# Kernel tuning notes

Measured on AMD Instinct MI355X. Metric: run time of the kernel, lower is better.

The kernel has to match this reference:

```python
import jax, jax.numpy as jnp
import numpy as np

B, S, D_MODEL, H = 2, 2048, 2048, 16
HEAD_DIM = D_MODEL // H  # 128


def setup_inputs() -> dict:
    key = jax.random.key(0)
    k1, k2, k3 = jax.random.split(key, 3)
    x = jax.random.normal(k1, (B, S, D_MODEL), dtype=jnp.float32)
    Wqkv = jax.random.normal(k2, (D_MODEL, 3 * D_MODEL), dtype=jnp.float32) * (D_MODEL ** -0.5)
    Wout = jax.random.normal(k3, (D_MODEL, D_MODEL), dtype=jnp.float32) * (D_MODEL ** -0.5)
    return {"x": x, "Wqkv": Wqkv, "Wout": Wout}


def reference(x, Wqkv, Wout):
    b, s, _ = x.shape
    # QKV projection: (B, S, 3*H*D) -> (B, S, 3, H, D)
    qkv = (x @ Wqkv).reshape(b, s, 3, H, HEAD_DIM)
    q, k, v = qkv[:, :, 0], qkv[:, :, 1], qkv[:, :, 2]
    scale = HEAD_DIM ** -0.5
    # scores: (B, H, Sq, Sk)
    scores = jnp.einsum("bqhd,bkhd->bhqk", q, k) * scale
    causal = jnp.arange(s)[:, None] >= jnp.arange(s)[None, :]
    scores = jnp.where(causal[None, None, :, :], scores, -1e9)
    attn = jax.nn.softmax(scores, axis=-1)
    out = jnp.einsum("bhqk,bkhd->bqhd", attn, v)  # (B, S, H, D)
    out = out.reshape(b, s, D_MODEL)
    return out @ Wout
```

## Files before the change

### kernel.cpp

```cpp
#include <hip/hip_runtime.h>
#include <hip/hip_bf16.h>


#define SEQ 2048
#define DM 2048
#define NQKV 6144
#define DH 128

typedef __attribute__((ext_vector_type(8))) short bf16x8;
typedef __attribute__((ext_vector_type(4))) float f32x4;

__device__ __forceinline__ f32x4 mfma16(bf16x8 a, bf16x8 b, f32x4 c) {
  return __builtin_amdgcn_mfma_f32_16x16x32_bf16(a, b, c, 0, 0, 0);
}

__device__ __forceinline__ void gload_lds16(const void* g, void* l) {
  __builtin_amdgcn_global_load_lds(
      (const __attribute__((address_space(1))) unsigned int*)g,
      (__attribute__((address_space(3))) unsigned int*)l, 16, 0, 0);
}

__global__ __launch_bounds__(256) void cast_f32_bf16(
    const float* __restrict__ in, __hip_bfloat16* __restrict__ out, int n4) {
  int i = blockIdx.x * 256 + threadIdx.x;
  if (i >= n4) return;
  float4 f = reinterpret_cast<const float4*>(in)[i];
  union { __hip_bfloat16 h[4]; unsigned long long u; } o;
  o.h[0] = __float2bfloat16(f.x); o.h[1] = __float2bfloat16(f.y);
  o.h[2] = __float2bfloat16(f.z); o.h[3] = __float2bfloat16(f.w);
  reinterpret_cast<unsigned long long*>(out)[i] = o.u;
}

__global__ __launch_bounds__(256) void transpose_cast(
    const float* __restrict__ in, __hip_bfloat16* __restrict__ out, int R, int C) {
  __shared__ float t[32][33];
  int c0 = blockIdx.x * 32, r0 = blockIdx.y * 32;
  int tx = threadIdx.x, ty = threadIdx.y;
#pragma unroll
  for (int i = 0; i < 4; ++i)
    t[ty + i * 8][tx] = in[(size_t)(r0 + ty + i * 8) * C + c0 + tx];
  __syncthreads();
#pragma unroll
  for (int i = 0; i < 4; ++i)
    out[(size_t)(c0 + ty + i * 8) * R + r0 + tx] = __float2bfloat16(t[tx][ty + i * 8]);
}

__global__ __launch_bounds__(256) void transpose_v(
    const __hip_bfloat16* __restrict__ qkv, __hip_bfloat16* __restrict__ vT) {
  __shared__ __hip_bfloat16 t[32][33];
  int bh = blockIdx.z;
  int b = bh >> 4, h = bh & 15;
  int s0 = blockIdx.x * 32, d0 = blockIdx.y * 32;
  int tx = threadIdx.x, ty = threadIdx.y;
#pragma unroll
  for (int i = 0; i < 4; ++i)
    t[ty + i * 8][tx] =
        qkv[(size_t)(b * SEQ + s0 + ty + i * 8) * NQKV + 2 * DM + h * DH + d0 + tx];
  __syncthreads();
#pragma unroll
  for (int i = 0; i < 4; ++i)
    vT[(size_t)(bh * DH + d0 + ty + i * 8) * SEQ + s0 + tx] = t[tx][ty + i * 8];
}

template <int EPI>
__global__ __launch_bounds__(256) void gemm_bt(
    const __hip_bfloat16* __restrict__ A, const __hip_bfloat16* __restrict__ Bt,
    void* __restrict__ Cout, int M, int N, int K) {
  __shared__ alignas(16) __hip_bfloat16 As[128 * 64];
  __shared__ alignas(16) __hip_bfloat16 Bs[128 * 64];
  const int tid = threadIdx.x;
  const int lane = tid & 63;
  const int w = tid >> 6, wr = w >> 1, wc = w & 1;
  const int lr = lane & 15, lg = lane >> 4;
  const int m0 = blockIdx.y * 128, n0 = blockIdx.x * 128;
  f32x4 acc[4][4] = {};
  for (int k0 = 0; k0 < K; k0 += 64) {
#pragma unroll
    for (int it = 0; it < 4; ++it) {
      int e = (it * 256 + tid) * 8;
      int row = e >> 6, col = e & 63;
      gload_lds16(A + (size_t)(m0 + row) * K + k0 + col, (char*)As + (size_t)e * 2);
      gload_lds16(Bt + (size_t)(n0 + row) * K + k0 + col, (char*)Bs + (size_t)e * 2);
    }
    __syncthreads();
#pragma unroll
    for (int ks = 0; ks < 2; ++ks) {
      bf16x8 af[4], bfr[4];
#pragma unroll
      for (int m = 0; m < 4; ++m)
        af[m] = *(const bf16x8*)((const char*)As +
                                 (wr * 64 + m * 16 + lr) * 128 + ks * 64 + lg * 16);
#pragma unroll
      for (int n = 0; n < 4; ++n)
        bfr[n] = *(const bf16x8*)((const char*)Bs +
                                  (wc * 64 + n * 16 + lr) * 128 + ks * 64 + lg * 16);
#pragma unroll
      for (int m = 0; m < 4; ++m)
#pragma unroll
        for (int n = 0; n < 4; ++n)
          acc[m][n] = mfma16(af[m], bfr[n], acc[m][n]);
    }
    __syncthreads();
  }
  const int crow = m0 + wr * 64, ccol = n0 + wc * 64;
#pragma unroll
  for (int m = 0; m < 4; ++m)
#pragma unroll
    for (int n = 0; n < 4; ++n)
#pragma unroll
      for (int j = 0; j < 4; ++j) {
        int r = crow + m * 16 + lg * 4 + j;
        int c = ccol + n * 16 + lr;
        if (EPI == 0)
          ((__hip_bfloat16*)Cout)[(size_t)r * N + c] = __float2bfloat16(acc[m][n][j]);
        else
          ((float*)Cout)[(size_t)r * N + c] = acc[m][n][j];
      }
}

__global__ __launch_bounds__(256) void attn_causal(
    const __hip_bfloat16* __restrict__ qkv, const __hip_bfloat16* __restrict__ vT,
    __hip_bfloat16* __restrict__ O) {
  __shared__ alignas(16) __hip_bfloat16 Ks[64 * 128];
  __shared__ alignas(16) __hip_bfloat16 Vs[128 * 64];
  __shared__ alignas(16) __hip_bfloat16 Ps[4][16 * 64];
  const int tid = threadIdx.x, lane = tid & 63, w = tid >> 6;
  const int lr = lane & 15, lg = lane >> 4;
  const int qt = blockIdx.x, bh = blockIdx.y;
  const int b = bh >> 4, h = bh & 15;
  const int q0 = qt * 64;
  const int qrow = q0 + w * 16 + lr;
  const __hip_bfloat16* qp = qkv + (size_t)(b * SEQ + qrow) * NQKV + h * DH;
  bf16x8 qf[4];
#pragma unroll
  for (int ks = 0; ks < 4; ++ks) qf[ks] = *(const bf16x8*)(qp + ks * 32 + lg * 8);
  f32x4 of[8] = {};
  float mrun[4], lrun[4];
#pragma unroll
  for (int j = 0; j < 4; ++j) { mrun[j] = -1e30f; lrun[j] = 0.f; }
  const float scale = 0.08838834764831845f;
  const int myq = q0 + w * 16 + lg * 4;

  for (int t = 0; t <= qt; ++t) {
    const int kv0 = t * 64;
#pragma unroll
    for (int it = 0; it < 4; ++it) {
      int g = it * 256 + tid;
      int r = g >> 4, sl = g & 15;
      int ssl = sl ^ (r & 7);
      gload_lds16(qkv + (size_t)(b * SEQ + kv0 + r) * NQKV + DM + h * DH + ssl * 8,
                  (char*)Ks + (size_t)g * 16);
    }
#pragma unroll
    for (int it = 0; it < 4; ++it) {
      int g = it * 256 + tid;
      int r = g >> 3, sl = g & 7;
      int ssl = sl ^ (r & 7);
      gload_lds16(vT + (size_t)(bh * DH + r) * SEQ + kv0 + ssl * 8,
                  (char*)Vs + (size_t)g * 16);
    }
    __syncthreads();

    f32x4 sacc[4] = {};
#pragma unroll
    for (int n = 0; n < 4; ++n) {
      const int krow = n * 16 + lr;
      const char* kbase = (const char*)Ks + krow * 256;
#pragma unroll
      for (int ks = 0; ks < 4; ++ks) {
        int c = ks * 64 + lg * 16;
        bf16x8 kb = *(const bf16x8*)(kbase + (c ^ ((krow & 7) << 4)));
        sacc[n] = mfma16(qf[ks], kb, sacc[n]);
      }
    }
    const bool dg = (t == qt);
#pragma unroll
    for (int n = 0; n < 4; ++n)
#pragma unroll
      for (int j = 0; j < 4; ++j) {
        float v = sacc[n][j] * scale;
        if (dg && (kv0 + n * 16 + lr > myq + j)) v = -1e30f;
        sacc[n][j] = v;
      }
    float pm[4];
#pragma unroll
    for (int j = 0; j < 4; ++j)
      pm[j] = fmaxf(fmaxf(sacc[0][j], sacc[1][j]), fmaxf(sacc[2][j], sacc[3][j]));
#pragma unroll
    for (int d = 1; d < 16; d <<= 1)
#pragma unroll
      for (int j = 0; j < 4; ++j) pm[j] = fmaxf(pm[j], __shfl_xor(pm[j], d));
    float corr[4], rs[4];
#pragma unroll
    for (int j = 0; j < 4; ++j) {
      float mn = fmaxf(mrun[j], pm[j]);
      corr[j] = __expf(mrun[j] - mn);
      mrun[j] = mn;
      rs[j] = 0.f;
    }
#pragma unroll
    for (int n = 0; n < 4; ++n)
#pragma unroll
      for (int j = 0; j < 4; ++j) {
        float p = __expf(sacc[n][j] - mrun[j]);
        sacc[n][j] = p;
        rs[j] += p;
      }
#pragma unroll
    for (int d = 1; d < 16; d <<= 1)
#pragma unroll
      for (int j = 0; j < 4; ++j) rs[j] += __shfl_xor(rs[j], d);
#pragma unroll
    for (int j = 0; j < 4; ++j) lrun[j] = lrun[j] * corr[j] + rs[j];
#pragma unroll
    for (int nn = 0; nn < 8; ++nn)
#pragma unroll
      for (int j = 0; j < 4; ++j) of[nn][j] *= corr[j];

    __hip_bfloat16* pw = &Ps[w][0];
#pragma unroll
    for (int j = 0; j < 4; ++j) {
      int prow = lg * 4 + j;
      char* pb = (char*)pw + prow * 128;
#pragma unroll
      for (int n = 0; n < 4; ++n) {
        int c = (n * 16 + lr) * 2;
        *(__hip_bfloat16*)(pb + (c ^ ((prow & 7) << 4))) = __float2bfloat16(sacc[n][j]);
      }
    }
#pragma unroll
    for (int kvs = 0; kvs < 2; ++kvs) {
      int c = kvs * 64 + lg * 16;
      bf16x8 pa = *(const bf16x8*)((const char*)pw + lr * 128 + (c ^ ((lr & 7) << 4)));
#pragma unroll
      for (int nn = 0; nn < 8; ++nn) {
        int vrow = nn * 16 + lr;
        bf16x8 vb =
            *(const bf16x8*)((const char*)Vs + vrow * 128 + (c ^ ((vrow & 7) << 4)));
        of[nn] = mfma16(pa, vb, of[nn]);
      }
    }
    __syncthreads();
  }
#pragma unroll
  for (int j = 0; j < 4; ++j) {
    float inv = 1.0f / lrun[j];
    size_t orow = (size_t)(b * SEQ + q0 + w * 16 + lg * 4 + j);
    __hip_bfloat16* op = O + orow * DM + h * DH;
#pragma unroll
    for (int nn = 0; nn < 8; ++nn)
      op[nn * 16 + lr] = __float2bfloat16(of[nn][j] * inv);
  }
}

extern "C" void kernel_launch(void* const* d_in, const int* in_sizes, int n_in,
                              void* d_out, int out_size, void* d_ws, size_t ws_size,
                              hipStream_t stream) {
  const float* x = (const float*)d_in[0];
  const float* Wqkv = (const float*)d_in[1];
  const float* Wout = (const float*)d_in[2];
  float* out = (float*)d_out;
  char* ws = (char*)d_ws;
  __hip_bfloat16* xb    = (__hip_bfloat16*)(ws + 0);
  __hip_bfloat16* wqkvT = (__hip_bfloat16*)(ws + (size_t)16777216);
  __hip_bfloat16* woutT = (__hip_bfloat16*)(ws + (size_t)41943040);
  __hip_bfloat16* qkvb  = (__hip_bfloat16*)(ws + (size_t)50331648);
  __hip_bfloat16* vT    = (__hip_bfloat16*)(ws + (size_t)100663296);
  __hip_bfloat16* ob    = (__hip_bfloat16*)(ws + (size_t)117440512);

  cast_f32_bf16<<<dim3(8192), dim3(256), 0, stream>>>(x, xb, 8388608 / 4);
  transpose_cast<<<dim3(192, 64), dim3(32, 8), 0, stream>>>(Wqkv, wqkvT, 2048, 6144);
  transpose_cast<<<dim3(64, 64), dim3(32, 8), 0, stream>>>(Wout, woutT, 2048, 2048);
  gemm_bt<0><<<dim3(48, 32), dim3(256), 0, stream>>>(xb, wqkvT, qkvb, 4096, 6144, 2048);
  transpose_v<<<dim3(64, 4, 32), dim3(32, 8), 0, stream>>>(qkvb, vT);
  attn_causal<<<dim3(32, 32), dim3(256), 0, stream>>>(qkvb, vT, ob);
  gemm_bt<1><<<dim3(16, 32), dim3(256), 0, stream>>>(ob, woutT, out, 4096, 2048, 2048);
}
```

Baseline: 507.3 us.

## Pair causal query tiles per block, widen KV tiles, add lazy rescale

Each attention block now handles two query tiles (p and 31-p), so the causal work is balanced across blocks and each K/V tile loaded into LDS is shared by both query tiles. KV tiles grow from 64 to 128 rows, and the grid halves to 16x32 blocks. Online softmax rescaling is skipped unless the row max rises by more than 8, which cuts exp and multiply work on the accumulators. In exchange the kernel uses more LDS and registers, has fewer blocks to fill the GPU, and does extra masked work on the half-empty diagonal 128-wide tile.

```diff
diff --git a/kernel.cpp b/kernel.cpp
--- a/kernel.cpp
+++ b/kernel.cpp
@@ -118,33 +118,133 @@
       }
 }
 
-__global__ __launch_bounds__(256) void attn_causal(
+__device__ __forceinline__ void attn_tile(
+    const bf16x8 (&qf)[4], f32x4 (&of)[8], float (&mrun)[4], float (&lrun)[4],
+    const char* Ks, const char* Vs, char* pw,
+    int lr, int lg, int kv0, int myq, bool lastmask, float scale) {
+  f32x4 sacc[8];
+#pragma unroll
+  for (int n = 0; n < 8; ++n) sacc[n] = f32x4{0.f, 0.f, 0.f, 0.f};
+#pragma unroll
+  for (int n = 0; n < 8; ++n) {
+    const int krow = n * 16 + lr;
+    const char* kbase = Ks + krow * 256;
+#pragma unroll
+    for (int ks = 0; ks < 4; ++ks) {
+      int c = ks * 64 + lg * 16;
+      bf16x8 kb = *(const bf16x8*)(kbase + (c ^ ((krow & 7) << 4)));
+      sacc[n] = mfma16(qf[ks], kb, sacc[n]);
+    }
+  }
+#pragma unroll
+  for (int n = 0; n < 8; ++n)
+#pragma unroll
+    for (int j = 0; j < 4; ++j) {
+      float v = sacc[n][j] * scale;
+      if (lastmask && (kv0 + n * 16 + lr > myq + j)) v = -1e30f;
+      sacc[n][j] = v;
+    }
+  float pm[4];
+#pragma unroll
+  for (int j = 0; j < 4; ++j) {
+    float a = fmaxf(fmaxf(sacc[0][j], sacc[1][j]), fmaxf(sacc[2][j], sacc[3][j]));
+    float bx = fmaxf(fmaxf(sacc[4][j], sacc[5][j]), fmaxf(sacc[6][j], sacc[7][j]));
+    pm[j] = fmaxf(a, bx);
+  }
+#pragma unroll
+  for (int d = 1; d < 16; d <<= 1)
+#pragma unroll
+    for (int j = 0; j < 4; ++j) pm[j] = fmaxf(pm[j], __shfl_xor(pm[j], d));
+  bool big = false;
+#pragma unroll
+  for (int j = 0; j < 4; ++j) big = big || (pm[j] > mrun[j] + 8.0f);
+  if (__any(big)) {
+#pragma unroll
+    for (int j = 0; j < 4; ++j) {
+      float mn = fmaxf(mrun[j], pm[j]);
+      float corr = __expf(mrun[j] - mn);
+      mrun[j] = mn;
+      lrun[j] *= corr;
+#pragma unroll
+      for (int nn = 0; nn < 8; ++nn) of[nn][j] *= corr;
+    }
+  }
+  float rs[4] = {0.f, 0.f, 0.f, 0.f};
+#pragma unroll
+  for (int n = 0; n < 8; ++n)
+#pragma unroll
+    for (int j = 0; j < 4; ++j) {
+      float pv = __expf(sacc[n][j] - mrun[j]);
+      sacc[n][j] = pv;
+      rs[j] += pv;
+    }
+#pragma unroll
+  for (int d = 1; d < 16; d <<= 1)
+#pragma unroll
+    for (int j = 0; j < 4; ++j) rs[j] += __shfl_xor(rs[j], d);
+#pragma unroll
+  for (int j = 0; j < 4; ++j) lrun[j] += rs[j];
+#pragma unroll
+  for (int j = 0; j < 4; ++j) {
+    int prow = lg * 4 + j;
+    char* pb = pw + prow * 256;
+#pragma unroll
+    for (int n = 0; n < 8; ++n) {
+      int c = (n * 16 + lr) * 2;
+      *(__hip_bfloat16*)(pb + (c ^ ((prow & 7) << 4))) = __float2bfloat16(sacc[n][j]);
+    }
+  }
+#pragma unroll
+  for (int kvs = 0; kvs < 4; ++kvs) {
+    int c = kvs * 64 + lg * 16;
+    bf16x8 pa = *(const bf16x8*)(pw + lr * 256 + (c ^ ((lr & 7) << 4)));
+#pragma unroll
+    for (int nn = 0; nn < 8; ++nn) {
+      int vrow = nn * 16 + lr;
+      bf16x8 vb = *(const bf16x8*)(Vs + vrow * 256 + (c ^ ((vrow & 7) << 4)));
+      of[nn] = mfma16(pa, vb, of[nn]);
+    }
+  }
+}
+
+__global__ __launch_bounds__(256, 2) void attn_causal(
     const __hip_bfloat16* __restrict__ qkv, const __hip_bfloat16* __restrict__ vT,
     __hip_bfloat16* __restrict__ O) {
-  __shared__ alignas(16) __hip_bfloat16 Ks[64 * 128];
-  __shared__ alignas(16) __hip_bfloat16 Vs[128 * 64];
-  __shared__ alignas(16) __hip_bfloat16 Ps[4][16 * 64];
+  __shared__ alignas(16) __hip_bfloat16 Ks[128 * 128];
+  __shared__ alignas(16) __hip_bfloat16 Vs[128 * 128];
+  __shared__ alignas(16) __hip_bfloat16 Ps[4][16 * 128];
   const int tid = threadIdx.x, lane = tid & 63, w = tid >> 6;
   const int lr = lane & 15, lg = lane >> 4;
-  const int qt = blockIdx.x, bh = blockIdx.y;
+  const int p = blockIdx.x, bh = blockIdx.y;
   const int b = bh >> 4, h = bh & 15;
-  const int q0 = qt * 64;
-  const int qrow = q0 + w * 16 + lr;
-  const __hip_bfloat16* qp = qkv + (size_t)(b * SEQ + qrow) * NQKV + h * DH;
-  bf16x8 qf[4];
-#pragma unroll
-  for (int ks = 0; ks < 4; ++ks) qf[ks] = *(const bf16x8*)(qp + ks * 32 + lg * 8);
-  f32x4 of[8] = {};
-  float mrun[4], lrun[4];
-#pragma unroll
-  for (int j = 0; j < 4; ++j) { mrun[j] = -1e30f; lrun[j] = 0.f; }
+  const int qtA = p, qtB = 31 - p;
+  const int q0A = qtA * 64, q0B = qtB * 64;
+  const int ntA = (qtA + 2) >> 1, ntB = (qtB + 2) >> 1;
   const float scale = 0.08838834764831845f;
-  const int myq = q0 + w * 16 + lg * 4;
-
-  for (int t = 0; t <= qt; ++t) {
-    const int kv0 = t * 64;
-#pragma unroll
-    for (int it = 0; it < 4; ++it) {
+  bf16x8 qfA[4], qfB[4];
+  {
+    const __hip_bfloat16* qpA =
+        qkv + (size_t)(b * SEQ + q0A + w * 16 + lr) * NQKV + h * DH;
+    const __hip_bfloat16* qpB =
+        qkv + (size_t)(b * SEQ + q0B + w * 16 + lr) * NQKV + h * DH;
+#pragma unroll
+    for (int ks = 0; ks < 4; ++ks) {
+      qfA[ks] = *(const bf16x8*)(qpA + ks * 32 + lg * 8);
+      qfB[ks] = *(const bf16x8*)(qpB + ks * 32 + lg * 8);
+    }
+  }
+  f32x4 ofA[8] = {}, ofB[8] = {};
+  float mA[4], lA[4], mB[4], lB[4];
+#pragma unroll
+  for (int j = 0; j < 4; ++j) { mA[j] = mB[j] = -1e30f; lA[j] = lB[j] = 0.f; }
+  const int myqA = q0A + w * 16 + lg * 4;
+  const int myqB = q0B + w * 16 + lg * 4;
+  char* pw = (char*)&Ps[w][0];
+
+  for (int t = 0; t < ntB; ++t) {
+    const int kv0 = t * 128;
+#pragma unroll
+    for (int it = 0; it < 8; ++it) {
       int g = it * 256 + tid;
       int r = g >> 4, sl = g & 15;
       int ssl = sl ^ (r & 7);
@@ -152,104 +252,33 @@
                   (char*)Ks + (size_t)g * 16);
     }
 #pragma unroll
-    for (int it = 0; it < 4; ++it) {
+    for (int it = 0; it < 8; ++it) {
       int g = it * 256 + tid;
-      int r = g >> 3, sl = g & 7;
+      int r = g >> 4, sl = g & 15;
       int ssl = sl ^ (r & 7);
       gload_lds16(vT + (size_t)(bh * DH + r) * SEQ + kv0 + ssl * 8,
                   (char*)Vs + (size_t)g * 16);
     }
     __syncthreads();
-
-    f32x4 sacc[4] = {};
-#pragma unroll
-    for (int n = 0; n < 4; ++n) {
-      const int krow = n * 16 + lr;
-      const char* kbase = (const char*)Ks + krow * 256;
-#pragma unroll
-      for (int ks = 0; ks < 4; ++ks) {
-        int c = ks * 64 + lg * 16;
-        bf16x8 kb = *(const bf16x8*)(kbase + (c ^ ((krow & 7) << 4)));
-        sacc[n] = mfma16(qf[ks], kb, sacc[n]);
-      }
-    }
-    const bool dg = (t == qt);
-#pragma unroll
-    for (int n = 0; n < 4; ++n)
-#pragma unroll
-      for (int j = 0; j < 4; ++j) {
-        float v = sacc[n][j] * scale;
-        if (dg && (kv0 + n * 16 + lr > myq + j)) v = -1e30f;
-        sacc[n][j] = v;
-      }
-    float pm[4];
-#pragma unroll
-    for (int j = 0; j < 4; ++j)
-      pm[j] = fmaxf(fmaxf(sacc[0][j], sacc[1][j]), fmaxf(sacc[2][j], sacc[3][j]));
-#pragma unroll
-    for (int d = 1; d < 16; d <<= 1)
-#pragma unroll
-      for (int j = 0; j < 4; ++j) pm[j] = fmaxf(pm[j], __shfl_xor(pm[j], d));
-    float corr[4], rs[4];
-#pragma unroll
-    for (int j = 0; j < 4; ++j) {
-      float mn = fmaxf(mrun[j], pm[j]);
-      corr[j] = __expf(mrun[j] - mn);
-      mrun[j] = mn;
-      rs[j] = 0.f;
-    }
-#pragma unroll
-    for (int n = 0; n < 4; ++n)
-#pragma unroll
-      for (int j = 0; j < 4; ++j) {
-        float p = __expf(sacc[n][j] - mrun[j]);
-        sacc[n][j] = p;
-        rs[j] += p;
-      }
-#pragma unroll
-    for (int d = 1; d < 16; d <<= 1)
-#pragma unroll
-      for (int j = 0; j < 4; ++j) rs[j] += __shfl_xor(rs[j], d);
-#pragma unroll
-    for (int j = 0; j < 4; ++j) lrun[j] = lrun[j] * corr[j] + rs[j];
-#pragma unroll
-    for (int nn = 0; nn < 8; ++nn)
-#pragma unroll
-      for (int j = 0; j < 4; ++j) of[nn][j] *= corr[j];
-
-    __hip_bfloat16* pw = &Ps[w][0];
-#pragma unroll
-    for (int j = 0; j < 4; ++j) {
-      int prow = lg * 4 + j;
-      char* pb = (char*)pw + prow * 128;
-#pragma unroll
-      for (int n = 0; n < 4; ++n) {
-        int c = (n * 16 + lr) * 2;
-        *(__hip_bfloat16*)(pb + (c ^ ((prow & 7) << 4))) = __float2bfloat16(sacc[n][j]);
-      }
-    }
-#pragma unroll
-    for (int kvs = 0; kvs < 2; ++kvs) {
-      int c = kvs * 64 + lg * 16;
-      bf16x8 pa = *(const bf16x8*)((const char*)pw + lr * 128 + (c ^ ((lr & 7) << 4)));
-#pragma unroll
-      for (int nn = 0; nn < 8; ++nn) {
-        int vrow = nn * 16 + lr;
-        bf16x8 vb =
-            *(const bf16x8*)((const char*)Vs + vrow * 128 + (c ^ ((vrow & 7) << 4)));
-        of[nn] = mfma16(pa, vb, of[nn]);
-      }
-    }
+    if (t < ntA)
+      attn_tile(qfA, ofA, mA, lA, (const char*)Ks, (const char*)Vs, pw,
+                lr, lg, kv0, myqA, t == ntA - 1, scale);
+    attn_tile(qfB, ofB, mB, lB, (const char*)Ks, (const char*)Vs, pw,
+              lr, lg, kv0, myqB, t == ntB - 1, scale);
     __syncthreads();
   }
 #pragma unroll
   for (int j = 0; j < 4; ++j) {
-    float inv = 1.0f / lrun[j];
-    size_t orow = (size_t)(b * SEQ + q0 + w * 16 + lg * 4 + j);
-    __hip_bfloat16* op = O + orow * DM + h * DH;
-#pragma unroll
-    for (int nn = 0; nn < 8; ++nn)
-      op[nn * 16 + lr] = __float2bfloat16(of[nn][j] * inv);
+    float invA = 1.0f / lA[j], invB = 1.0f / lB[j];
+    __hip_bfloat16* opA =
+        O + (size_t)(b * SEQ + q0A + w * 16 + lg * 4 + j) * DM + h * DH;
+    __hip_bfloat16* opB =
+        O + (size_t)(b * SEQ + q0B + w * 16 + lg * 4 + j) * DM + h * DH;
+#pragma unroll
+    for (int nn = 0; nn < 8; ++nn) {
+      opA[nn * 16 + lr] = __float2bfloat16(ofA[nn][j] * invA);
+      opB[nn * 16 + lr] = __float2bfloat16(ofB[nn][j] * invB);
+    }
   }
 }
 
@@ -273,6 +302,6 @@
   transpose_cast<<<dim3(64, 64), dim3(32, 8), 0, stream>>>(Wout, woutT, 2048, 2048);
   gemm_bt<0><<<dim3(48, 32), dim3(256), 0, stream>>>(xb, wqkvT, qkvb, 4096, 6144, 2048);
   transpose_v<<<dim3(64, 4, 32), dim3(32, 8), 0, stream>>>(qkvb, vT);
-  attn_causal<<<dim3(32, 32), dim3(256), 0, stream>>>(qkvb, vT, ob);
+  attn_causal<<<dim3(16, 32), dim3(256), 0, stream>>>(qkvb, vT, ob);
   gemm_bt<1><<<dim3(16, 32), dim3(256), 0, stream>>>(ob, woutT, out, 4096, 2048, 2048);
 }
```

Result: faster. 435.2 us (-14.2%).
